# Kernel tuning notes

Measured on AMD Instinct MI355X. Metric: run time of the kernel, lower is better.

The kernel has to match this reference:

```python
import jax, jax.numpy as jnp
import numpy as np

D_MODEL = 2048
NUM_HEADS = 16
D_FF = 8192
EPS = 1e-5


def setup_inputs() -> dict:
    key = jax.random.key(0)
    ks = jax.random.split(key, 9)
    s = 0.02
    return {
        "x": jax.random.normal(ks[0], (2, 2048, D_MODEL), dtype=jnp.float32),
        "wq": jax.random.normal(ks[1], (D_MODEL, D_MODEL), dtype=jnp.float32) * s,
        "wk": jax.random.normal(ks[2], (D_MODEL, D_MODEL), dtype=jnp.float32) * s,
        "wv": jax.random.normal(ks[3], (D_MODEL, D_MODEL), dtype=jnp.float32) * s,
        "wo": jax.random.normal(ks[4], (D_MODEL, D_MODEL), dtype=jnp.float32) * s,
        "w1": jax.random.normal(ks[5], (D_FF, D_MODEL), dtype=jnp.float32) * s,
        "w2": jax.random.normal(ks[6], (D_MODEL, D_FF), dtype=jnp.float32) * s,
        "g1": jnp.ones((D_MODEL,), dtype=jnp.float32),
        "g2": jnp.ones((D_MODEL,), dtype=jnp.float32),
    }


def rmsnorm(a, g):
    rms = jnp.sqrt(jnp.sum(a * a, axis=-1, keepdims=True) / a.shape[-1] + EPS)
    return a / rms * g


def attention(xn, wq, wk, wv, wo):
    B, S, D = xn.shape
    H, dk = NUM_HEADS, D // NUM_HEADS
    # Linear weights are (out, in); y = x @ W^T
    q = (xn @ wq.T).reshape(B, S, H, dk).transpose(0, 2, 1, 3)  # bhsd
    k = (xn @ wk.T).reshape(B, S, H, dk).transpose(0, 2, 1, 3)
    v = (xn @ wv.T).reshape(B, S, H, dk).transpose(0, 2, 1, 3)
    scores = jnp.einsum("bhqd,bhkd->bhqk", q, k) * (dk ** -0.5)
    causal = jnp.triu(jnp.ones((S, S), dtype=bool), k=1)
    scores = jnp.where(causal, -jnp.inf, scores)
    probs = jax.nn.softmax(scores, axis=-1)
    out = jnp.einsum("bhqk,bhkd->bhqd", probs, v)
    out = out.transpose(0, 2, 1, 3).reshape(B, S, D)
    return out @ wo.T


def reference(x, wq, wk, wv, wo, w1, w2, g1, g2):
    x = x + attention(rmsnorm(x, g1), wq, wk, wv, wo)
    h = jax.nn.gelu(rmsnorm(x, g2) @ w1.T, approximate=False)
    x = x + h @ w2.T
    return x
```

## Files before the change

kernel.cpp:

```cpp
#include <hip/hip_runtime.h>
#include <hip/hip_bf16.h>
#include <math.h>

#define D_MODEL 2048
#define SEQ     2048
#define BATCH   2
#define NHEAD   16
#define DK      128
#define DFF     8192
#define MROWS   (BATCH*SEQ)

typedef short short8 __attribute__((ext_vector_type(8)));
typedef float f32x4  __attribute__((ext_vector_type(4)));

__device__ __forceinline__ short f2bf(float f) {
  union { __hip_bfloat16 b; short s; } u;
  u.b = __float2bfloat16(f);
  return u.s;
}

#define MF(a, b, c) __builtin_amdgcn_mfma_f32_16x16x32_bf16(a, b, c, 0, 0, 0)
#define STG(gptr, ldsbyte) { \
    unsigned _m0v = (unsigned)__builtin_amdgcn_readfirstlane((int)(ldsbyte)); \
    asm volatile("s_mov_b32 m0, %1\n\tglobal_load_lds_dwordx4 %0, off" \
                 :: "v"(gptr), "s"(_m0v) : "memory"); }

__global__ __launch_bounds__(256) void rmsnorm_k(const float* __restrict__ x,
                                                 const float* __restrict__ g,
                                                 short* __restrict__ o) {
  const int row = blockIdx.x;
  const int t = threadIdx.x;
  const float4* xr = (const float4*)(x + (size_t)row * D_MODEL);
  const float4* gr = (const float4*)g;
  float4 v0 = xr[2*t], v1 = xr[2*t+1];
  float s = v0.x*v0.x + v0.y*v0.y + v0.z*v0.z + v0.w*v0.w
          + v1.x*v1.x + v1.y*v1.y + v1.z*v1.z + v1.w*v1.w;
  #pragma unroll
  for (int off = 1; off < 64; off <<= 1) s += __shfl_xor(s, off);
  __shared__ float red[4];
  if ((t & 63) == 0) red[t >> 6] = s;
  __syncthreads();
  float tot = red[0] + red[1] + red[2] + red[3];
  float inv = rsqrtf(tot * (1.0f / D_MODEL) + 1e-5f);
  float4 g0 = gr[2*t], g1v = gr[2*t+1];
  short8 ov;
  ov[0] = f2bf(v0.x * inv * g0.x);
  ov[1] = f2bf(v0.y * inv * g0.y);
  ov[2] = f2bf(v0.z * inv * g0.z);
  ov[3] = f2bf(v0.w * inv * g0.w);
  ov[4] = f2bf(v1.x * inv * g1v.x);
  ov[5] = f2bf(v1.y * inv * g1v.y);
  ov[6] = f2bf(v1.z * inv * g1v.z);
  ov[7] = f2bf(v1.w * inv * g1v.w);
  *((short8*)(o + (size_t)row * D_MODEL) + t) = ov;
}

__global__ __launch_bounds__(256) void f2b_k(const float* __restrict__ src,
                                             short* __restrict__ dst, int n8) {
  int i = blockIdx.x * 256 + threadIdx.x;
  if (i >= n8) return;
  const float4* s4 = (const float4*)src + 2 * (size_t)i;
  float4 a = s4[0], b = s4[1];
  short8 o = { f2bf(a.x), f2bf(a.y), f2bf(a.z), f2bf(a.w),
               f2bf(b.x), f2bf(b.y), f2bf(b.z), f2bf(b.w) };
  *((short8*)dst + i) = o;
}

__global__ __launch_bounds__(256) void combine_k(const float* p0, const float* p1,
                                                 const float* r, float* o, int n4) {
  int i = blockIdx.x * 256 + threadIdx.x;
  if (i >= n4) return;
  const float4 a = ((const float4*)p0)[i];
  const float4 b = ((const float4*)p1)[i];
  const float4 c = ((const float4*)r)[i];
  float4 d;
  d.x = a.x + b.x + c.x; d.y = a.y + b.y + c.y;
  d.z = a.z + b.z + c.z; d.w = a.w + b.w + c.w;
  ((float4*)o)[i] = d;
}

template<int EPI, int SPLIT>
__global__ __launch_bounds__(512, 2) void gemm256(const short* __restrict__ A,
                                                  const short* __restrict__ Bp,
                                                  void* Cv,
                                                  const float* __restrict__ resid,
                                                  int M, int N, int K,
                                                  int lda, int ldb, int nbx) {
  __shared__ __align__(16) short As[2][2][128 * 64];
  __shared__ __align__(16) short Bs[2][2][128 * 64];
  const int nk = K >> 6;
  const int cpx = gridDim.x >> 3;
  const int lin = (blockIdx.x & 7) * cpx + (blockIdx.x >> 3);
  const int bx = lin % nbx;
  int row2 = lin / nbx, by, ks = 0;
  if (SPLIT) { ks = row2 & 1; by = row2 >> 1; } else { by = row2; }
  const int m0 = bx * 256, n0 = by * 256;
  if (SPLIT) { A += (size_t)ks * K; Bp += (size_t)ks * K; }

  const int t = threadIdx.x, w = t >> 6, lane = t & 63, lr = lane & 15, lg = lane >> 4;
  const int wm = w >> 2, wn = w & 3;
  const unsigned aByte = (unsigned)(size_t)(const __attribute__((address_space(3))) short*)&As[0][0][0];
  const unsigned bByte = (unsigned)(size_t)(const __attribute__((address_space(3))) short*)&Bs[0][0][0];
  const unsigned wOff = (unsigned)(w * 1024);

  const int r = t >> 3, c8 = t & 7;
  const int sw = (c8 ^ (r & 7)) << 3;
  const short* pA0 = A  + (size_t)(m0 + r)       * lda + sw;
  const short* pA1 = A  + (size_t)(m0 + 128 + r) * lda + sw;
  const short* pB0 = Bp + (size_t)(n0 + r)       * ldb + sw;
  const short* pB1 = Bp + (size_t)(n0 + 128 + r) * ldb + sw;
  const size_t l64A = (size_t)64 * lda, l64B = (size_t)64 * ldb;

#define STAGE_TILE(tt, slotByteA, slotByteB) { \
    const short* a0_ = pA0 + (size_t)(tt) * 64; \
    STG(a0_, (slotByteA) + wOff);            STG(a0_ + l64A, (slotByteA) + 8192u + wOff); \
    const short* a1_ = pA1 + (size_t)(tt) * 64; \
    STG(a1_, (slotByteA) + 16384u + wOff);   STG(a1_ + l64A, (slotByteA) + 16384u + 8192u + wOff); \
    const short* b0_ = pB0 + (size_t)(tt) * 64; \
    STG(b0_, (slotByteB) + wOff);            STG(b0_ + l64B, (slotByteB) + 8192u + wOff); \
    const short* b1_ = pB1 + (size_t)(tt) * 64; \
    STG(b1_, (slotByteB) + 16384u + wOff);   STG(b1_ + l64B, (slotByteB) + 16384u + 8192u + wOff); }

  f32x4 acc[8][4];
  const f32x4 z4 = {0.f, 0.f, 0.f, 0.f};
  #pragma unroll
  for (int m = 0; m < 8; ++m)
    #pragma unroll
    for (int n = 0; n < 4; ++n) acc[m][n] = z4;

  STAGE_TILE(0, aByte, bByte);
  asm volatile("s_waitcnt vmcnt(0)" ::: "memory");
  __builtin_amdgcn_s_barrier();

  for (int T = 0; T < nk; ++T) {
    const int p = T & 1, q = p ^ 1;

    if (T + 1 < nk)
      STAGE_TILE(T + 1, aByte + (unsigned)q * 32768u, bByte + (unsigned)q * 32768u);

    short8 bk0[4], bk1[4], aA[4];
    #pragma unroll
    for (int n = 0; n < 4; ++n) {
      int br = wn * 64 + n * 16 + lr;
      const short* bp = &Bs[p][br >> 7][(br & 127) * 64];
      bk0[n] = *(const short8*)&bp[(lg * 8) ^ ((br & 7) << 3)];
    }
    #pragma unroll
    for (int m = 0; m < 4; ++m) {
      int ar = m * 16 + lr;
      aA[m] = *(const short8*)&As[p][wm][ar * 64 + ((lg * 8) ^ ((ar & 7) << 3))];
    }
    #pragma unroll
    for (int m = 0; m < 4; ++m)
      #pragma unroll
      for (int n = 0; n < 4; ++n) acc[m][n] = MF(aA[m], bk0[n], acc[m][n]);

    short8 aB[4];
    #pragma unroll
    for (int m = 0; m < 4; ++m) {
      int ar = 64 + m * 16 + lr;
      aB[m] = *(const short8*)&As[p][wm][ar * 64 + ((lg * 8) ^ ((ar & 7) << 3))];
    }
    #pragma unroll
    for (int m = 0; m < 4; ++m)
      #pragma unroll
      for (int n = 0; n < 4; ++n) acc[m + 4][n] = MF(aB[m], bk0[n], acc[m + 4][n]);

    short8 aC[4];
    #pragma unroll
    for (int n = 0; n < 4; ++n) {
      int br = wn * 64 + n * 16 + lr;
      const short* bp = &Bs[p][br >> 7][(br & 127) * 64];
      bk1[n] = *(const short8*)&bp[(32 + lg * 8) ^ ((br & 7) << 3)];
    }
    #pragma unroll
    for (int m = 0; m < 4; ++m) {
      int ar = m * 16 + lr;
      aC[m] = *(const short8*)&As[p][wm][ar * 64 + ((32 + lg * 8) ^ ((ar & 7) << 3))];
    }
    #pragma unroll
    for (int m = 0; m < 4; ++m)
      #pragma unroll
      for (int n = 0; n < 4; ++n) acc[m][n] = MF(aC[m], bk1[n], acc[m][n]);

    short8 aD[4];
    #pragma unroll
    for (int m = 0; m < 4; ++m) {
      int ar = 64 + m * 16 + lr;
      aD[m] = *(const short8*)&As[p][wm][ar * 64 + ((32 + lg * 8) ^ ((ar & 7) << 3))];
    }
    #pragma unroll
    for (int m = 0; m < 4; ++m)
      #pragma unroll
      for (int n = 0; n < 4; ++n) acc[m + 4][n] = MF(aD[m], bk1[n], acc[m + 4][n]);

    if (T + 1 < nk) {
      asm volatile("s_waitcnt vmcnt(0)" ::: "memory");
      __builtin_amdgcn_s_barrier();
    }
  }
#undef STAGE_TILE

  float* Cf = (float*)Cv;
  if (SPLIT) Cf += (size_t)ks * ((size_t)M * N);
  #pragma unroll
  for (int m = 0; m < 8; ++m)
    #pragma unroll
    for (int n = 0; n < 4; ++n)
      #pragma unroll
      for (int rr = 0; rr < 4; ++rr) {
        int row = m0 + wm * 128 + m * 16 + lg * 4 + rr;
        int col = n0 + wn * 64 + n * 16 + lr;
        size_t idx = (size_t)row * N + col;
        float vv = acc[m][n][rr];
        if (EPI == 0) {
          ((short*)Cv)[idx] = f2bf(vv);
        } else if (EPI == 1) {
          float gl = 0.5f * vv * (1.0f + erff(vv * 0.70710678118654752f));
          ((short*)Cv)[idx] = f2bf(gl);
        } else if (EPI == 2) {
          ((float*)Cv)[idx] = vv + resid[idx];
        } else {
          Cf[idx] = vv;
        }
      }
}

__global__ __launch_bounds__(256) void vtrans(const short* __restrict__ QKV,
                                              short* __restrict__ VT) {
  const int st = blockIdx.x;
  const int bh = blockIdx.y;
  const int b = bh >> 4, h = bh & 15;
  const int t = threadIdx.x;
  __shared__ __align__(16) short T[64 * 128];
  const short* Vsrc = QKV + ((size_t)b * SEQ) * 6144 + 2 * D_MODEL + h * DK;
  {
    int r = t >> 4, c = (t & 15) * 8;
    #pragma unroll
    for (int i = 0; i < 4; ++i) {
      int rr = r + 16 * i;
      uint4 vv = *(const uint4*)(Vsrc + (size_t)(st * 64 + rr) * 6144 + c);
      *(uint4*)&T[rr * 128 + (c ^ (((rr >> 3) & 7) << 3))] = vv;
    }
  }
  __syncthreads();
  short* dst = VT + ((size_t)bh * DK) * SEQ + st * 64;
  {
    int c2 = (t & 7) * 8;
    #pragma unroll
    for (int i = 0; i < 4; ++i) {
      int d = (t >> 3) + 32 * i;
      short8 ov;
      #pragma unroll
      for (int j = 0; j < 8; ++j)
        ov[j] = T[(c2 + j) * 128 + (d ^ ((((c2 + j) >> 3) & 7) << 3))];
      *(short8*)(dst + (size_t)d * SEQ + c2) = ov;
    }
  }
}

__global__ __launch_bounds__(512, 2) void attn3(const short* __restrict__ QKV,
                                                const short* __restrict__ VT,
                                                short* __restrict__ O) {
  const float SC = 0.12751743f;
  const int a = blockIdx.x, bh = blockIdx.y;
  const int b = bh >> 4, h = bh & 15;
  const int t = threadIdx.x, w = t >> 6, lane = t & 63, lr = lane & 15, lg = lane >> 4;
  const short* Qp = QKV + ((size_t)b * SEQ) * 6144 + h * DK;
  const short* Kp = Qp + D_MODEL;
  const short* Vp = VT + ((size_t)bh * DK) * SEQ;
  __shared__ __align__(16) short Ks[2][64 * 128];
  __shared__ __align__(16) short Vs[2][128 * 64];
  __shared__ __align__(16) short Ps[8][16][72];

  const int krr = t >> 4, kcc = (t & 15) * 8;
  const int vdd = t >> 3, vcc = (t & 7) * 8;
  const f32x4 z4 = {0.f, 0.f, 0.f, 0.f};

  for (int sub = 0; sub < 2; ++sub) {
    const int ts = sub ? (15 - a) : a;
    const int nt = 2 * ts + 2;
    const int qrow0 = ts * 128 + w * 16;

    short8 qf[4];
    #pragma unroll
    for (int ki = 0; ki < 4; ++ki)
      qf[ki] = *(const short8*)(Qp + (size_t)(qrow0 + lr) * 6144 + ki * 32 + lg * 8);

    f32x4 acc[8];
    #pragma unroll
    for (int nd = 0; nd < 8; ++nd) acc[nd] = z4;
    float mrow[4], lsum[4];
    #pragma unroll
    for (int r = 0; r < 4; ++r) { mrow[r] = -INFINITY; lsum[r] = 0.f; }

    uint4 krg[2], vrg[2];
    #pragma unroll
    for (int i = 0; i < 2; ++i) {
      krg[i] = *(const uint4*)(Kp + (size_t)(krr + 32 * i) * 6144 + kcc);
      vrg[i] = *(const uint4*)(Vp + (size_t)(vdd + 64 * i) * SEQ + vcc);
    }
    __syncthreads();
    #pragma unroll
    for (int i = 0; i < 2; ++i) {
      int r = krr + 32 * i;
      *(uint4*)&Ks[0][(r * 128 + kcc) ^ ((r & 7) << 3)] = krg[i];
      int d = vdd + 64 * i;
      *(uint4*)&Vs[0][(d * 64 + vcc) ^ ((d & 7) << 3)] = vrg[i];
    }
    __syncthreads();

    int cur = 0;
    for (int tt = 0; tt < nt; ++tt) {
      const bool pre = (tt + 1 < nt);
      if (pre) {
        #pragma unroll
        for (int i = 0; i < 2; ++i) {
          krg[i] = *(const uint4*)(Kp + (size_t)((tt + 1) * 64 + krr + 32 * i) * 6144 + kcc);
          vrg[i] = *(const uint4*)(Vp + (size_t)(vdd + 64 * i) * SEQ + (tt + 1) * 64 + vcc);
        }
      }

      f32x4 sf[4] = {z4, z4, z4, z4};
      #pragma unroll
      for (int ki = 0; ki < 4; ++ki) {
        #pragma unroll
        for (int nk = 0; nk < 4; ++nk) {
          int rr = nk * 16 + lr;
          short8 kf = *(const short8*)&Ks[cur][(rr * 128 + ki * 32 + lg * 8) ^ ((rr & 7) << 3)];
          sf[nk] = MF(qf[ki], kf, sf[nk]);
        }
      }

      const bool diag = (tt * 64 + 63 > qrow0);
      #pragma unroll
      for (int r = 0; r < 4; ++r) {
        int qg = qrow0 + lg * 4 + r;
        float s0 = sf[0][r] * SC, s1 = sf[1][r] * SC, s2 = sf[2][r] * SC, s3 = sf[3][r] * SC;
        if (diag) {
          int c0 = tt * 64 + lr;
          s0 = (c0      <= qg) ? s0 : -3.0e38f;
          s1 = (c0 + 16 <= qg) ? s1 : -3.0e38f;
          s2 = (c0 + 32 <= qg) ? s2 : -3.0e38f;
          s3 = (c0 + 48 <= qg) ? s3 : -3.0e38f;
        }
        float mx = fmaxf(fmaxf(s0, s1), fmaxf(s2, s3));
        mx = fmaxf(mx, __shfl_xor(mx, 1));
        mx = fmaxf(mx, __shfl_xor(mx, 2));
        mx = fmaxf(mx, __shfl_xor(mx, 4));
        mx = fmaxf(mx, __shfl_xor(mx, 8));
        float mnew = fmaxf(mrow[r], mx);
        float alpha = exp2f(mrow[r] - mnew);
        mrow[r] = mnew;
        float p0 = exp2f(s0 - mnew), p1 = exp2f(s1 - mnew),
              p2 = exp2f(s2 - mnew), p3 = exp2f(s3 - mnew);
        lsum[r] = lsum[r] * alpha + ((p0 + p1) + (p2 + p3));
        #pragma unroll
        for (int nd = 0; nd < 8; ++nd) acc[nd][r] *= alpha;
        short* pr = &Ps[w][lg * 4 + r][0];
        pr[lr]      = f2bf(p0);
        pr[16 + lr] = f2bf(p1);
        pr[32 + lr] = f2bf(p2);
        pr[48 + lr] = f2bf(p3);
      }
      asm volatile("s_waitcnt lgkmcnt(0)" ::: "memory");
      __builtin_amdgcn_sched_barrier(0);

      short8 pf0 = *(const short8*)&Ps[w][lr][lg * 8];
      short8 pf1 = *(const short8*)&Ps[w][lr][32 + lg * 8];
      #pragma unroll
      for (int nd = 0; nd < 8; ++nd) {
        int rr = nd * 16 + lr;
        short8 vf0 = *(const short8*)&Vs[cur][(rr * 64 + lg * 8) ^ ((rr & 7) << 3)];
        short8 vf1 = *(const short8*)&Vs[cur][(rr * 64 + 32 + lg * 8) ^ ((rr & 7) << 3)];
        acc[nd] = MF(pf0, vf0, acc[nd]);
        acc[nd] = MF(pf1, vf1, acc[nd]);
      }
      __syncthreads();
      if (pre) {
        #pragma unroll
        for (int i = 0; i < 2; ++i) {
          int r = krr + 32 * i;
          *(uint4*)&Ks[cur ^ 1][(r * 128 + kcc) ^ ((r & 7) << 3)] = krg[i];
          int d = vdd + 64 * i;
          *(uint4*)&Vs[cur ^ 1][(d * 64 + vcc) ^ ((d & 7) << 3)] = vrg[i];
        }
      }
      __syncthreads();
      cur ^= 1;
    }

    float inv[4];
    #pragma unroll
    for (int r = 0; r < 4; ++r) {
      float ls = lsum[r];
      ls += __shfl_xor(ls, 1);
      ls += __shfl_xor(ls, 2);
      ls += __shfl_xor(ls, 4);
      ls += __shfl_xor(ls, 8);
      inv[r] = 1.0f / ls;
    }
    #pragma unroll
    for (int nd = 0; nd < 8; ++nd)
      #pragma unroll
      for (int r = 0; r < 4; ++r) {
        int row = qrow0 + lg * 4 + r;
        O[(size_t)(b * SEQ + row) * D_MODEL + h * DK + nd * 16 + lr] = f2bf(acc[nd][r] * inv[r]);
      }
  }
}

template<int EPI>
__global__ __launch_bounds__(256) void gemm_bt(const short* __restrict__ A,
                                               const float* __restrict__ B,
                                               void* Cv,
                                               const float* resid,
                                               int M, int N, int K) {
  __shared__ __align__(16) short As[128][72];
  __shared__ __align__(16) short Bs[128][72];
  const int t = threadIdx.x;
  const int m0 = blockIdx.x * 128, n0 = blockIdx.y * 128;
  const int wave = t >> 6, lane = t & 63, lr = lane & 15, lg = lane >> 4;
  const int wr = (wave >> 1) * 64, wc = (wave & 1) * 64;

  f32x4 acc[4][4];
  const f32x4 z4 = {0.f, 0.f, 0.f, 0.f};
  #pragma unroll
  for (int m = 0; m < 4; ++m)
    #pragma unroll
    for (int n = 0; n < 4; ++n) acc[m][n] = z4;

  int ar[4], ac[4];
  #pragma unroll
  for (int i = 0; i < 4; ++i) { int u = t + 256*i; ar[i] = u >> 3; ac[i] = (u & 7) * 8; }

  for (int k0 = 0; k0 < K; k0 += 64) {
    #pragma unroll
    for (int i = 0; i < 4; ++i) {
      uint4 va = *(const uint4*)(A + (size_t)(m0 + ar[i]) * K + k0 + ac[i]);
      *(uint4*)&As[ar[i]][ac[i]] = va;
    }
    #pragma unroll
    for (int i = 0; i < 4; ++i) {
      const float4* bp = (const float4*)(B + (size_t)(n0 + ar[i]) * K + k0 + ac[i]);
      float4 b0 = bp[0], b1 = bp[1];
      short8 pb = { f2bf(b0.x), f2bf(b0.y), f2bf(b0.z), f2bf(b0.w),
                    f2bf(b1.x), f2bf(b1.y), f2bf(b1.z), f2bf(b1.w) };
      *(short8*)&Bs[ar[i]][ac[i]] = pb;
    }
    __syncthreads();
    #pragma unroll
    for (int kk = 0; kk < 64; kk += 32) {
      short8 af[4], bfr[4];
      #pragma unroll
      for (int m = 0; m < 4; ++m) af[m]  = *(const short8*)&As[wr + m*16 + lr][kk + lg*8];
      #pragma unroll
      for (int n = 0; n < 4; ++n) bfr[n] = *(const short8*)&Bs[wc + n*16 + lr][kk + lg*8];
      #pragma unroll
      for (int m = 0; m < 4; ++m)
        #pragma unroll
        for (int n = 0; n < 4; ++n)
          acc[m][n] = MF(af[m], bfr[n], acc[m][n]);
    }
    __syncthreads();
  }

  #pragma unroll
  for (int m = 0; m < 4; ++m)
    #pragma unroll
    for (int n = 0; n < 4; ++n)
      #pragma unroll
      for (int r = 0; r < 4; ++r) {
        int row = m0 + wr + m*16 + lg*4 + r;
        int col = n0 + wc + n*16 + lr;
        size_t idx = (size_t)row * N + col;
        float vv = acc[m][n][r];
        if (EPI == 0) {
          ((short*)Cv)[idx] = f2bf(vv);
        } else if (EPI == 1) {
          float gl = 0.5f * vv * (1.0f + erff(vv * 0.70710678118654752f));
          ((short*)Cv)[idx] = f2bf(gl);
        } else {
          ((float*)Cv)[idx] = vv + resid[idx];
        }
      }
}

__global__ __launch_bounds__(256) void attn_k(const short* __restrict__ Q,
                                              const short* __restrict__ K,
                                              const short* __restrict__ V,
                                              short* __restrict__ O) {
  const float scale = 0.08838834764831845f;
  const int qt = blockIdx.x;
  const int bh = blockIdx.y;
  const int b = bh >> 4, h = bh & 15;
  const size_t base = ((size_t)b * SEQ) * D_MODEL + (size_t)h * DK;
  const int t = threadIdx.x, wave = t >> 6, lane = t & 63, lr = lane & 15, lg = lane >> 4;

  __shared__ __align__(16) short Ks[32][136];
  __shared__ __align__(16) short Vt[128][40];
  __shared__ __align__(16) short Ps[4][32][40];

  const int qrow0 = qt * 128 + wave * 32;
  short8 qf[2][4];
  #pragma unroll
  for (int mq = 0; mq < 2; ++mq)
    #pragma unroll
    for (int ki = 0; ki < 4; ++ki)
      qf[mq][ki] = *(const short8*)(Q + base + (size_t)(qrow0 + mq*16 + lr) * D_MODEL + ki*32 + lg*8);

  f32x4 acc[2][8];
  const f32x4 z4 = {0.f, 0.f, 0.f, 0.f};
  #pragma unroll
  for (int mq = 0; mq < 2; ++mq)
    #pragma unroll
    for (int nd = 0; nd < 8; ++nd) acc[mq][nd] = z4;
  float mrow[2][4], lsum[2][4];
  #pragma unroll
  for (int mq = 0; mq < 2; ++mq)
    #pragma unroll
    for (int r = 0; r < 4; ++r) { mrow[mq][r] = -INFINITY; lsum[mq][r] = 0.f; }

  const int lastt = qt * 4 + 3;
  for (int tt = 0; tt <= lastt; ++tt) {
    #pragma unroll
    for (int i = 0; i < 2; ++i) {
      int u = t + 256*i; int r = u >> 4; int c = (u & 15) * 8;
      *(uint4*)&Ks[r][c] = *(const uint4*)(K + base + (size_t)(tt*32 + r) * D_MODEL + c);
      uint4 vv = *(const uint4*)(V + base + (size_t)(tt*32 + r) * D_MODEL + c);
      const short* sv = (const short*)&vv;
      #pragma unroll
      for (int j = 0; j < 8; ++j) Vt[c + j][r] = sv[j];
    }
    __syncthreads();
    if (tt <= qt * 4 + wave) {
      f32x4 sf[2][2] = {{z4, z4}, {z4, z4}};
      #pragma unroll
      for (int ki = 0; ki < 4; ++ki) {
        short8 kf0 = *(const short8*)&Ks[lr][ki*32 + lg*8];
        short8 kf1 = *(const short8*)&Ks[16 + lr][ki*32 + lg*8];
        sf[0][0] = MF(qf[0][ki], kf0, sf[0][0]);
        sf[0][1] = MF(qf[0][ki], kf1, sf[0][1]);
        sf[1][0] = MF(qf[1][ki], kf0, sf[1][0]);
        sf[1][1] = MF(qf[1][ki], kf1, sf[1][1]);
      }
      #pragma unroll
      for (int mq = 0; mq < 2; ++mq) {
        #pragma unroll
        for (int r = 0; r < 4; ++r) {
          int qg = qrow0 + mq*16 + lg*4 + r;
          float s0 = sf[mq][0][r] * scale;
          float s1 = sf[mq][1][r] * scale;
          if (tt*32 + lr > qg)       s0 = -INFINITY;
          if (tt*32 + 16 + lr > qg)  s1 = -INFINITY;
          float mx = fmaxf(s0, s1);
          mx = fmaxf(mx, __shfl_xor(mx, 1));
          mx = fmaxf(mx, __shfl_xor(mx, 2));
          mx = fmaxf(mx, __shfl_xor(mx, 4));
          mx = fmaxf(mx, __shfl_xor(mx, 8));
          float mnew = fmaxf(mrow[mq][r], mx);
          float alpha = __expf(mrow[mq][r] - mnew);
          mrow[mq][r] = mnew;
          float p0 = __expf(s0 - mnew);
          float p1 = __expf(s1 - mnew);
          float ps = p0 + p1;
          ps += __shfl_xor(ps, 1);
          ps += __shfl_xor(ps, 2);
          ps += __shfl_xor(ps, 4);
          ps += __shfl_xor(ps, 8);
          lsum[mq][r] = lsum[mq][r] * alpha + ps;
          #pragma unroll
          for (int nd = 0; nd < 8; ++nd) acc[mq][nd][r] *= alpha;
          Ps[wave][mq*16 + lg*4 + r][lr]      = f2bf(p0);
          Ps[wave][mq*16 + lg*4 + r][16 + lr] = f2bf(p1);
        }
      }
      asm volatile("s_waitcnt lgkmcnt(0)" ::: "memory");
      short8 pf0 = *(const short8*)&Ps[wave][lr][lg*8];
      short8 pf1 = *(const short8*)&Ps[wave][16 + lr][lg*8];
      #pragma unroll
      for (int nd = 0; nd < 8; ++nd) {
        short8 vf = *(const short8*)&Vt[nd*16 + lr][lg*8];
        acc[0][nd] = MF(pf0, vf, acc[0][nd]);
        acc[1][nd] = MF(pf1, vf, acc[1][nd]);
      }
    }
    __syncthreads();
  }

  #pragma unroll
  for (int mq = 0; mq < 2; ++mq)
    #pragma unroll
    for (int nd = 0; nd < 8; ++nd)
      #pragma unroll
      for (int r = 0; r < 4; ++r) {
        int row = qrow0 + mq*16 + lg*4 + r;
        O[base + (size_t)row * D_MODEL + nd*16 + lr] = f2bf(acc[mq][nd][r] / lsum[mq][r]);
      }
}

extern "C" void kernel_launch(void* const* d_in, const int* in_sizes, int n_in,
                              void* d_out, int out_size, void* d_ws, size_t ws_size,
                              hipStream_t stream) {
  const float* x  = (const float*)d_in[0];
  const float* wq = (const float*)d_in[1];
  const float* wk = (const float*)d_in[2];
  const float* wv = (const float*)d_in[3];
  const float* wo = (const float*)d_in[4];
  const float* w1 = (const float*)d_in[5];
  const float* w2 = (const float*)d_in[6];
  const float* g1 = (const float*)d_in[7];
  const float* g2 = (const float*)d_in[8];
  float* out = (float*)d_out;
  char* ws = (char*)d_ws;

  const size_t NEED = (size_t)192 << 20;
  if (ws_size >= NEED) {
    short* wqkv = (short*)(ws);
    short* wo_b = (short*)(ws + ((size_t)24 << 20));
    short* w1_b = (short*)(ws + ((size_t)32 << 20));
    short* w2_b = (short*)(ws + ((size_t)64 << 20));
    short* qkv  = (short*)(ws + ((size_t)96 << 20));
    short* vt   = (short*)(ws + ((size_t)144 << 20));
    short* ab   = (short*)(ws + ((size_t)160 << 20));
    short* xn   = (short*)(ws + ((size_t)176 << 20));
    short* hb   = (short*)(ws + ((size_t)96 << 20));
    float* pf   = (float*)(ws + ((size_t)160 << 20));

    const int NW = D_MODEL * D_MODEL / 8;
    f2b_k<<<(NW + 255) / 256, 256, 0, stream>>>(wq, wqkv,                   NW);
    f2b_k<<<(NW + 255) / 256, 256, 0, stream>>>(wk, wqkv + (size_t)D_MODEL * D_MODEL,     NW);
    f2b_k<<<(NW + 255) / 256, 256, 0, stream>>>(wv, wqkv + (size_t)2 * D_MODEL * D_MODEL, NW);
    f2b_k<<<(NW + 255) / 256, 256, 0, stream>>>(wo, wo_b, NW);
    const int NF = DFF * D_MODEL / 8;
    f2b_k<<<(NF + 255) / 256, 256, 0, stream>>>(w1, w1_b, NF);
    f2b_k<<<(NF + 255) / 256, 256, 0, stream>>>(w2, w2_b, NF);

    rmsnorm_k<<<MROWS, 256, 0, stream>>>(x, g1, xn);
    gemm256<0,0><<<dim3(16 * 24), 512, 0, stream>>>(xn, wqkv, qkv, nullptr,
                                                    MROWS, 6144, D_MODEL, D_MODEL, D_MODEL, 16);
    vtrans<<<dim3(SEQ/64, BATCH*NHEAD), 256, 0, stream>>>(qkv, vt);
    attn3<<<dim3(8, BATCH*NHEAD), 512, 0, stream>>>(qkv, vt, ab);
    gemm256<2,0><<<dim3(16 * 8), 512, 0, stream>>>(ab, wo_b, out, x,
                                                   MROWS, D_MODEL, D_MODEL, D_MODEL, D_MODEL, 16);
    rmsnorm_k<<<MROWS, 256, 0, stream>>>(out, g2, xn);
    gemm256<1,0><<<dim3(16 * 32), 512, 0, stream>>>(xn, w1_b, hb, nullptr,
                                                    MROWS, DFF, D_MODEL, D_MODEL, D_MODEL, 16);
    gemm256<3,1><<<dim3(16 * 8 * 2), 512, 0, stream>>>(hb, w2_b, pf, nullptr,
                                                       MROWS, D_MODEL, DFF / 2, DFF, DFF, 16);
    const int N4 = MROWS * D_MODEL / 4;
    combine_k<<<(N4 + 255) / 256, 256, 0, stream>>>(pf, pf + (size_t)MROWS * D_MODEL, out, out, N4);
  } else {
    short* qb = (short*)(ws + ((size_t)0  << 20));
    short* kb = (short*)(ws + ((size_t)16 << 20));
    short* vb = (short*)(ws + ((size_t)32 << 20));
    short* ab = (short*)(ws + ((size_t)48 << 20));
    short* xn = (short*)(ws + ((size_t)64 << 20));
    short* hb = (short*)(ws + ((size_t)0  << 20));

    dim3 gproj(MROWS / 128, D_MODEL / 128);
    rmsnorm_k<<<MROWS, 256, 0, stream>>>(x, g1, xn);
    gemm_bt<0><<<gproj, 256, 0, stream>>>(xn, wq, qb, nullptr, MROWS, D_MODEL, D_MODEL);
    gemm_bt<0><<<gproj, 256, 0, stream>>>(xn, wk, kb, nullptr, MROWS, D_MODEL, D_MODEL);
    gemm_bt<0><<<gproj, 256, 0, stream>>>(xn, wv, vb, nullptr, MROWS, D_MODEL, D_MODEL);
    attn_k<<<dim3(SEQ / 128, BATCH * NHEAD), 256, 0, stream>>>(qb, kb, vb, ab);
    gemm_bt<2><<<gproj, 256, 0, stream>>>(ab, wo, out, x, MROWS, D_MODEL, D_MODEL);
    rmsnorm_k<<<MROWS, 256, 0, stream>>>(out, g2, xn);
    for (int half = 0; half < 2; ++half) {
      const short* xh = xn  + (size_t)half * 2048 * D_MODEL;
      float*       oh = out + (size_t)half * 2048 * D_MODEL;
      gemm_bt<1><<<dim3(2048 / 128, DFF / 128), 256, 0, stream>>>(xh, w1, hb, nullptr, 2048, DFF, D_MODEL);
      gemm_bt<2><<<dim3(2048 / 128, D_MODEL / 128), 256, 0, stream>>>(hb, w2, oh, oh, 2048, D_MODEL, DFF);
    }
  }
}
```

Measured before the change: 743.1 us.

## Switch GEMM to four-stage K=32 LDS pipeline with deeper prefetch

Restructures the 256x256 GEMM main loop from a double-buffered K=64 tile into a four-slot ring of K=32 tiles. Three tiles are prefetched ahead, and partial vmcnt waits let global-to-LDS loads overlap more compute. The goal is to hide memory latency better and keep the MFMA pipes busier with a single barrier per step. The XOR swizzle on the LDS layout is dropped, so the 64-byte row stride may cause LDS bank conflicts on the ds_read_b128 fragment loads. Per-iteration barrier and loop overhead also grow relative to the MFMA work.

```diff
diff --git a/kernel.cpp b/kernel.cpp
--- a/kernel.cpp
+++ b/kernel.cpp
@@ -86,9 +86,9 @@
                                                   const float* __restrict__ resid,
                                                   int M, int N, int K,
                                                   int lda, int ldb, int nbx) {
-  __shared__ __align__(16) short As[2][2][128 * 64];
-  __shared__ __align__(16) short Bs[2][2][128 * 64];
-  const int nk = K >> 6;
+  __shared__ __align__(16) short As[4][256 * 32];
+  __shared__ __align__(16) short Bs[4][256 * 32];
+  const int nk = K >> 5;
   const int cpx = gridDim.x >> 3;
   const int lin = (blockIdx.x & 7) * cpx + (blockIdx.x >> 3);
   const int bx = lin % nbx;
@@ -99,27 +99,22 @@
 
   const int t = threadIdx.x, w = t >> 6, lane = t & 63, lr = lane & 15, lg = lane >> 4;
   const int wm = w >> 2, wn = w & 3;
-  const unsigned aByte = (unsigned)(size_t)(const __attribute__((address_space(3))) short*)&As[0][0][0];
-  const unsigned bByte = (unsigned)(size_t)(const __attribute__((address_space(3))) short*)&Bs[0][0][0];
+  const unsigned aByte = (unsigned)(size_t)(const __attribute__((address_space(3))) short*)&As[0][0];
+  const unsigned bByte = (unsigned)(size_t)(const __attribute__((address_space(3))) short*)&Bs[0][0];
   const unsigned wOff = (unsigned)(w * 1024);
 
-  const int r = t >> 3, c8 = t & 7;
-  const int sw = (c8 ^ (r & 7)) << 3;
-  const short* pA0 = A  + (size_t)(m0 + r)       * lda + sw;
-  const short* pA1 = A  + (size_t)(m0 + 128 + r) * lda + sw;
-  const short* pB0 = Bp + (size_t)(n0 + r)       * ldb + sw;
-  const short* pB1 = Bp + (size_t)(n0 + 128 + r) * ldb + sw;
-  const size_t l64A = (size_t)64 * lda, l64B = (size_t)64 * ldb;
-
-#define STAGE_TILE(tt, slotByteA, slotByteB) { \
-    const short* a0_ = pA0 + (size_t)(tt) * 64; \
-    STG(a0_, (slotByteA) + wOff);            STG(a0_ + l64A, (slotByteA) + 8192u + wOff); \
-    const short* a1_ = pA1 + (size_t)(tt) * 64; \
-    STG(a1_, (slotByteA) + 16384u + wOff);   STG(a1_ + l64A, (slotByteA) + 16384u + 8192u + wOff); \
-    const short* b0_ = pB0 + (size_t)(tt) * 64; \
-    STG(b0_, (slotByteB) + wOff);            STG(b0_ + l64B, (slotByteB) + 8192u + wOff); \
-    const short* b1_ = pB1 + (size_t)(tt) * 64; \
-    STG(b1_, (slotByteB) + 16384u + wOff);   STG(b1_ + l64B, (slotByteB) + 16384u + 8192u + wOff); }
+  const int r = t >> 2, c8s = (t & 3) * 8;
+  const short* pA = A  + (size_t)(m0 + r) * lda + c8s;
+  const short* pB = Bp + (size_t)(n0 + r) * ldb + c8s;
+  const size_t l128A = (size_t)128 * lda, l128B = (size_t)128 * ldb;
+
+#define STAGE(tt, s) { \
+    const short* a_ = pA + (size_t)(tt) * 32; \
+    STG(a_, aByte + (unsigned)(s) * 16384u + wOff); \
+    STG(a_ + l128A, aByte + (unsigned)(s) * 16384u + 8192u + wOff); \
+    const short* b_ = pB + (size_t)(tt) * 32; \
+    STG(b_, bByte + (unsigned)(s) * 16384u + wOff); \
+    STG(b_ + l128B, bByte + (unsigned)(s) * 16384u + 8192u + wOff); }
 
   f32x4 acc[8][4];
   const f32x4 z4 = {0.f, 0.f, 0.f, 0.f};
@@ -128,78 +123,42 @@
     #pragma unroll
     for (int n = 0; n < 4; ++n) acc[m][n] = z4;
 
-  STAGE_TILE(0, aByte, bByte);
-  asm volatile("s_waitcnt vmcnt(0)" ::: "memory");
+#define COMPUTE(s) { \
+    short8 bf_[4], af_[8]; \
+    _Pragma("unroll") \
+    for (int n = 0; n < 4; ++n) { \
+      int br = wn * 64 + n * 16 + lr; \
+      bf_[n] = *(const short8*)&Bs[s][br * 32 + lg * 8]; \
+    } \
+    _Pragma("unroll") \
+    for (int m = 0; m < 8; ++m) { \
+      int ar = wm * 128 + m * 16 + lr; \
+      af_[m] = *(const short8*)&As[s][ar * 32 + lg * 8]; \
+    } \
+    _Pragma("unroll") \
+    for (int m = 0; m < 8; ++m) \
+      _Pragma("unroll") \
+      for (int n = 0; n < 4; ++n) acc[m][n] = MF(af_[m], bf_[n], acc[m][n]); }
+
+  STAGE(0, 0); STAGE(1, 1); STAGE(2, 2);
+  asm volatile("s_waitcnt vmcnt(8)" ::: "memory");
   __builtin_amdgcn_s_barrier();
 
-  for (int T = 0; T < nk; ++T) {
-    const int p = T & 1, q = p ^ 1;
-
-    if (T + 1 < nk)
-      STAGE_TILE(T + 1, aByte + (unsigned)q * 32768u, bByte + (unsigned)q * 32768u);
-
-    short8 bk0[4], bk1[4], aA[4];
-    #pragma unroll
-    for (int n = 0; n < 4; ++n) {
-      int br = wn * 64 + n * 16 + lr;
-      const short* bp = &Bs[p][br >> 7][(br & 127) * 64];
-      bk0[n] = *(const short8*)&bp[(lg * 8) ^ ((br & 7) << 3)];
-    }
-    #pragma unroll
-    for (int m = 0; m < 4; ++m) {
-      int ar = m * 16 + lr;
-      aA[m] = *(const short8*)&As[p][wm][ar * 64 + ((lg * 8) ^ ((ar & 7) << 3))];
-    }
-    #pragma unroll
-    for (int m = 0; m < 4; ++m)
-      #pragma unroll
-      for (int n = 0; n < 4; ++n) acc[m][n] = MF(aA[m], bk0[n], acc[m][n]);
-
-    short8 aB[4];
-    #pragma unroll
-    for (int m = 0; m < 4; ++m) {
-      int ar = 64 + m * 16 + lr;
-      aB[m] = *(const short8*)&As[p][wm][ar * 64 + ((lg * 8) ^ ((ar & 7) << 3))];
-    }
-    #pragma unroll
-    for (int m = 0; m < 4; ++m)
-      #pragma unroll
-      for (int n = 0; n < 4; ++n) acc[m + 4][n] = MF(aB[m], bk0[n], acc[m + 4][n]);
-
-    short8 aC[4];
-    #pragma unroll
-    for (int n = 0; n < 4; ++n) {
-      int br = wn * 64 + n * 16 + lr;
-      const short* bp = &Bs[p][br >> 7][(br & 127) * 64];
-      bk1[n] = *(const short8*)&bp[(32 + lg * 8) ^ ((br & 7) << 3)];
-    }
-    #pragma unroll
-    for (int m = 0; m < 4; ++m) {
-      int ar = m * 16 + lr;
-      aC[m] = *(const short8*)&As[p][wm][ar * 64 + ((32 + lg * 8) ^ ((ar & 7) << 3))];
-    }
-    #pragma unroll
-    for (int m = 0; m < 4; ++m)
-      #pragma unroll
-      for (int n = 0; n < 4; ++n) acc[m][n] = MF(aC[m], bk1[n], acc[m][n]);
-
-    short8 aD[4];
-    #pragma unroll
-    for (int m = 0; m < 4; ++m) {
-      int ar = 64 + m * 16 + lr;
-      aD[m] = *(const short8*)&As[p][wm][ar * 64 + ((32 + lg * 8) ^ ((ar & 7) << 3))];
-    }
-    #pragma unroll
-    for (int m = 0; m < 4; ++m)
-      #pragma unroll
-      for (int n = 0; n < 4; ++n) acc[m + 4][n] = MF(aD[m], bk1[n], acc[m + 4][n]);
-
-    if (T + 1 < nk) {
-      asm volatile("s_waitcnt vmcnt(0)" ::: "memory");
-      __builtin_amdgcn_s_barrier();
-    }
+  for (int T = 0; T < nk - 3; ++T) {
+    STAGE(T + 3, (T + 3) & 3);
+    COMPUTE(T & 3);
+    asm volatile("s_waitcnt vmcnt(8) lgkmcnt(0)" ::: "memory");
+    __builtin_amdgcn_s_barrier();
   }
-#undef STAGE_TILE
+  COMPUTE((nk - 3) & 3);
+  asm volatile("s_waitcnt vmcnt(4) lgkmcnt(0)" ::: "memory");
+  __builtin_amdgcn_s_barrier();
+  COMPUTE((nk - 2) & 3);
+  asm volatile("s_waitcnt vmcnt(0) lgkmcnt(0)" ::: "memory");
+  __builtin_amdgcn_s_barrier();
+  COMPUTE((nk - 1) & 3);
+#undef STAGE
+#undef COMPUTE
 
   float* Cf = (float*)Cv;
   if (SPLIT) Cf += (size_t)ks * ((size_t)M * N);
```

Result: slower. 800.4 us (+7.7%).
